# Kernel optimization log

Hardware: AMD Instinct MI355X
Metric: run time of the kernel (lower is better)

## Reference

```python
import jax, jax.numpy as jnp
import numpy as np

D_IN, D, TOPK = 64, 4, 12
SCALE = 1.0 / np.sqrt(np.float32(D_IN))


def setup_inputs() -> dict:
    key = jax.random.key(0)
    kx, kw = jax.random.split(key)
    x = jax.random.normal(kx, (8, 16, 512, D_IN), dtype=jnp.float32)
    flat = jax.random.normal(kw, (2 * D_IN * D,), dtype=jnp.float32)
    return {"x": x, "flat": flat}


def reference(x, flat):
    # x: (N, T, n, d_in); flat holds wk then wq, each (d_in, d)
    wk = flat[: D_IN * D].reshape(D_IN, D)
    wq = flat[D_IN * D :].reshape(D_IN, D)
    N, T, n, _ = x.shape
    k = jnp.einsum("btnc,cd->btnd", x, wk)  # (N,T,n,d)
    q = jnp.einsum("btnc,cd->btnd", x, wq)  # (N,T,n,d)
    # h = (X Wk)(X Wq)^T : h[i,j] = k_i . q_j -> (N,T,n,n)
    h = jnp.einsum("btnd,btmd->btnm", k, q)
    A = jax.nn.softmax(SCALE * h, axis=-1).sum(axis=-2)  # (N,T,n) column score sums
    # argsort descending + slice topk == top_k indices (values sorted descending)
    _, idxs = jax.lax.top_k(A, TOPK)  # (N,T,topk)
    return idxs.reshape(N, T, TOPK, 1)
```

## Files before the change

### kernel.cpp

```cpp
#include <hip/hip_runtime.h>
#include <math.h>

constexpr int kDIn  = 64;
constexpr int kN    = 512;
constexpr int kTopK = 12;
constexpr int kNBt  = 128;
constexpr int kS    = 4;
constexpr int kRows = kN / kS;
#define CEXP 0.18033688f
#define EXP2(v) __builtin_amdgcn_exp2f(v)
#define LOG2F(v) __builtin_amdgcn_logf(v)

#define DOT4(k, q)        fmaf((k).x,(q).x, fmaf((k).y,(q).y, fmaf((k).z,(q).z, (k).w*(q).w)))
#define DOT4A(k, q, add)  fmaf((k).x,(q).x, fmaf((k).y,(q).y, fmaf((k).z,(q).z, fmaf((k).w,(q).w,(add)))))

constexpr size_t kWsFloats = (size_t)kNBt * 16 * kN;

__global__ __launch_bounds__(512, 4) void fused_attn_kernel(
    const float* __restrict__ x, const float* __restrict__ flat,
    float* __restrict__ apart)
{
  __shared__ float4 Qs[kN];
  __shared__ float4 Ks[kRows];
  __shared__ float2 Pp[16 * kRows];
  __shared__ __align__(16) float Cs[kRows];

  const int tid  = threadIdx.x;
  const int p    = blockIdx.x;
  const int xcd  = p & 7;
  const int s    = (p >> 3) & 3;
  const int tile = ((p >> 5) << 3) | xcd;

  {
    const float4* fw  = reinterpret_cast<const float4*>(flat);
    const float4* xr4 = reinterpret_cast<const float4*>(x + ((size_t)tile * kN + tid) * kDIn);
    float4 xv[16];
#pragma unroll
    for (int i = 0; i < 16; ++i) xv[i] = xr4[i];

    float q0=0.f,q1=0.f,q2=0.f,q3=0.f;
    if ((tid >> 7) == s) {
      float k0=0.f,k1=0.f,k2=0.f,k3=0.f;
#pragma unroll
      for (int cc = 0; cc < 16; ++cc) {
#pragma unroll
        for (int u = 0; u < 4; ++u) {
          float v = (u==0)?xv[cc].x:(u==1)?xv[cc].y:(u==2)?xv[cc].z:xv[cc].w;
          float4 a = fw[cc*4+u];
          float4 b = fw[64 + cc*4+u];
          k0 = fmaf(v, a.x, k0); k1 = fmaf(v, a.y, k1);
          k2 = fmaf(v, a.z, k2); k3 = fmaf(v, a.w, k3);
          q0 = fmaf(v, b.x, q0); q1 = fmaf(v, b.y, q1);
          q2 = fmaf(v, b.z, q2); q3 = fmaf(v, b.w, q3);
        }
      }
      Ks[tid & 127] = make_float4(CEXP*k0, CEXP*k1, CEXP*k2, CEXP*k3);
    } else {
#pragma unroll
      for (int cc = 0; cc < 16; ++cc) {
#pragma unroll
        for (int u = 0; u < 4; ++u) {
          float v = (u==0)?xv[cc].x:(u==1)?xv[cc].y:(u==2)?xv[cc].z:xv[cc].w;
          float4 b = fw[64 + cc*4+u];
          q0 = fmaf(v, b.x, q0); q1 = fmaf(v, b.y, q1);
          q2 = fmaf(v, b.z, q2); q3 = fmaf(v, b.w, q3);
        }
      }
    }
    Qs[tid] = make_float4(q0, q1, q2, q3);
  }
  __syncthreads();

  {
    const int quad  = tid & 31;
    const int slice = tid >> 5;
    const float4 k0 = Ks[quad*4+0], k1 = Ks[quad*4+1];
    const float4 k2 = Ks[quad*4+2], k3 = Ks[quad*4+3];
    const float4* qb = &Qs[slice << 5];

    float m0=-INFINITY, m1=-INFINITY, m2=-INFINITY, m3=-INFINITY;
    float l0=0.f, l1=0.f, l2=0.f, l3=0.f;
#pragma unroll
    for (int c = 0; c < 32; c += 8) {
      float4 qv0 = qb[c+0], qv1 = qb[c+1], qv2 = qb[c+2], qv3 = qb[c+3];
      float4 qv4 = qb[c+4], qv5 = qb[c+5], qv6 = qb[c+6], qv7 = qb[c+7];
#define ROW_ONLINE(KR, MR, LR)                                                 \
      {                                                                        \
        float d0 = DOT4(KR, qv0), d1 = DOT4(KR, qv1);                          \
        float d2 = DOT4(KR, qv2), d3 = DOT4(KR, qv3);                          \
        float d4 = DOT4(KR, qv4), d5 = DOT4(KR, qv5);                          \
        float d6 = DOT4(KR, qv6), d7 = DOT4(KR, qv7);                          \
        float cm = fmaxf(fmaxf(fmaxf(d0,d1), fmaxf(d2,d3)),                    \
                         fmaxf(fmaxf(d4,d5), fmaxf(d6,d7)));                   \
        if (cm > MR) { LR *= EXP2(MR - cm); MR = cm; }                         \
        LR += ((EXP2(d0-MR) + EXP2(d1-MR)) + (EXP2(d2-MR) + EXP2(d3-MR)))      \
            + ((EXP2(d4-MR) + EXP2(d5-MR)) + (EXP2(d6-MR) + EXP2(d7-MR)));     \
      }
      ROW_ONLINE(k0, m0, l0)
      ROW_ONLINE(k1, m1, l1)
      ROW_ONLINE(k2, m2, l2)
      ROW_ONLINE(k3, m3, l3)
#undef ROW_ONLINE
    }
    float4* pp4 = reinterpret_cast<float4*>(&Pp[slice * kRows + quad*4]);
    pp4[0] = make_float4(m0, l0, m1, l1);
    pp4[1] = make_float4(m2, l2, m3, l3);
  }
  __syncthreads();

  if (tid < kRows) {
    float m = -INFINITY;
    float2 pr[16];
#pragma unroll
    for (int sl = 0; sl < 16; ++sl) {
      pr[sl] = Pp[sl * kRows + tid];
      m = fmaxf(m, pr[sl].x);
    }
    float l = 0.f;
#pragma unroll
    for (int sl = 0; sl < 16; ++sl) l += pr[sl].y * EXP2(pr[sl].x - m);
    Cs[tid] = m + LOG2F(l);
  }
  __syncthreads();

  {
    const int cq = tid & 127;
    const int rs = tid >> 7;
    const float4 q0 = Qs[cq*4+0], q1 = Qs[cq*4+1];
    const float4 q2 = Qs[cq*4+2], q3 = Qs[cq*4+3];
    const float4* kb = &Ks[rs << 5];
    const float4* cb = reinterpret_cast<const float4*>(&Cs[rs << 5]);

    float a0=0.f, a1=0.f, a2=0.f, a3=0.f;
#pragma unroll 2
    for (int ii = 0; ii < 8; ++ii) {
      float4 cc = cb[ii];
      float4 ka = kb[ii*4+0], kb_ = kb[ii*4+1], kc = kb[ii*4+2], kd = kb[ii*4+3];
      a0 += EXP2(DOT4A(q0, ka, -cc.x));  a1 += EXP2(DOT4A(q1, ka, -cc.x));
      a2 += EXP2(DOT4A(q2, ka, -cc.x));  a3 += EXP2(DOT4A(q3, ka, -cc.x));
      a0 += EXP2(DOT4A(q0, kb_, -cc.y)); a1 += EXP2(DOT4A(q1, kb_, -cc.y));
      a2 += EXP2(DOT4A(q2, kb_, -cc.y)); a3 += EXP2(DOT4A(q3, kb_, -cc.y));
      a0 += EXP2(DOT4A(q0, kc, -cc.z));  a1 += EXP2(DOT4A(q1, kc, -cc.z));
      a2 += EXP2(DOT4A(q2, kc, -cc.z));  a3 += EXP2(DOT4A(q3, kc, -cc.z));
      a0 += EXP2(DOT4A(q0, kd, -cc.w));  a1 += EXP2(DOT4A(q1, kd, -cc.w));
      a2 += EXP2(DOT4A(q2, kd, -cc.w));  a3 += EXP2(DOT4A(q3, kd, -cc.w));
    }
    reinterpret_cast<float4*>(apart + ((size_t)(tile*4 + s) * 4 + rs) * kN)[cq] =
        make_float4(a0, a1, a2, a3);
  }
}

__global__ __launch_bounds__(64) void topk_kernel(
    const float* __restrict__ apart, int* __restrict__ out)
{
  const int lane = threadIdx.x;
  const int bt   = blockIdx.x;
  const float* P = apart + (size_t)bt * 16 * kN;

  float v[8];
  {
    float4 acc0 = make_float4(0.f,0.f,0.f,0.f);
    float4 acc1 = make_float4(0.f,0.f,0.f,0.f);
#pragma unroll
    for (int sl = 0; sl < 16; ++sl) {
      const float4* Ps = reinterpret_cast<const float4*>(P + sl * kN);
      float4 u0 = Ps[lane*2], u1 = Ps[lane*2+1];
      acc0.x += u0.x; acc0.y += u0.y; acc0.z += u0.z; acc0.w += u0.w;
      acc1.x += u1.x; acc1.y += u1.y; acc1.z += u1.z; acc1.w += u1.w;
    }
    v[0]=acc0.x; v[1]=acc0.y; v[2]=acc0.z; v[3]=acc0.w;
    v[4]=acc1.x; v[5]=acc1.y; v[6]=acc1.z; v[7]=acc1.w;
  }

  for (int rnd = 0; rnd < kTopK; ++rnd) {
    float bv = v[0];
    int   bi = lane * 8;
#pragma unroll
    for (int r = 1; r < 8; ++r) {
      if (v[r] > bv) { bv = v[r]; bi = lane * 8 + r; }
    }
#pragma unroll
    for (int off = 32; off >= 1; off >>= 1) {
      float ov = __shfl_xor(bv, off);
      int   oi = __shfl_xor(bi, off);
      if (ov > bv || (ov == bv && oi < bi)) { bv = ov; bi = oi; }
    }
    if (lane == 0) out[bt * kTopK + rnd] = bi;
#pragma unroll
    for (int r = 0; r < 8; ++r) {
      if (lane * 8 + r == bi) v[r] = -INFINITY;
    }
  }
}

__global__ __launch_bounds__(512, 1) void sparse_attn_topk_fallback(
    const float* __restrict__ x, const float* __restrict__ flat, int* __restrict__ out)
{
  __shared__ float4 wk4[kDIn];
  __shared__ float4 wq4[kDIn];
  __shared__ float4 Ks[kN];
  __shared__ float4 Qs[kN];
  __shared__ float  Ms[kN];
  __shared__ float  Rl[kN];
  __shared__ float  As[kN];

  const int tid = threadIdx.x;
  const int bt  = blockIdx.x;

  if (tid < 64)       wk4[tid]      = reinterpret_cast<const float4*>(flat)[tid];
  else if (tid < 128) wq4[tid - 64] = reinterpret_cast<const float4*>(flat)[tid];
  __syncthreads();

  const float* xr = x + ((size_t)bt * kN + tid) * kDIn;
  float k0=0.f,k1=0.f,k2=0.f,k3=0.f, q0=0.f,q1=0.f,q2=0.f,q3=0.f;
#pragma unroll
  for (int c = 0; c < kDIn; ++c) {
    float xv = xr[c];
    float4 a = wk4[c];
    float4 b = wq4[c];
    k0 = fmaf(xv, a.x, k0); k1 = fmaf(xv, a.y, k1);
    k2 = fmaf(xv, a.z, k2); k3 = fmaf(xv, a.w, k3);
    q0 = fmaf(xv, b.x, q0); q1 = fmaf(xv, b.y, q1);
    q2 = fmaf(xv, b.z, q2); q3 = fmaf(xv, b.w, q3);
  }
  Ks[tid] = make_float4(k0, k1, k2, k3);
  Qs[tid] = make_float4(q0, q1, q2, q3);
  __syncthreads();

  float m = -INFINITY;
#pragma unroll 8
  for (int j = 0; j < kN; ++j) {
    float4 qj = Qs[j];
    float h = fmaf(k0, qj.x, fmaf(k1, qj.y, fmaf(k2, qj.z, k3 * qj.w)));
    m = fmaxf(m, h);
  }
  float l = 0.f;
#pragma unroll 8
  for (int j = 0; j < kN; ++j) {
    float4 qj = Qs[j];
    float h = fmaf(k0, qj.x, fmaf(k1, qj.y, fmaf(k2, qj.z, k3 * qj.w)));
    l += exp2f(CEXP * (h - m));
  }
  Ms[tid] = m;
  Rl[tid] = 1.0f / l;
  __syncthreads();

  float acc = 0.f;
#pragma unroll 8
  for (int i = 0; i < kN; ++i) {
    float4 ki = Ks[i];
    float h = fmaf(q0, ki.x, fmaf(q1, ki.y, fmaf(q2, ki.z, q3 * ki.w)));
    acc += exp2f(CEXP * (h - Ms[i])) * Rl[i];
  }
  As[tid] = acc;
  __syncthreads();

  if (tid < 64) {
    float v[8];
#pragma unroll
    for (int r = 0; r < 8; ++r) v[r] = As[tid * 8 + r];
    for (int rnd = 0; rnd < kTopK; ++rnd) {
      float bv = v[0];
      int   bi = tid * 8;
#pragma unroll
      for (int r = 1; r < 8; ++r)
        if (v[r] > bv) { bv = v[r]; bi = tid * 8 + r; }
#pragma unroll
      for (int off = 32; off >= 1; off >>= 1) {
        float ov = __shfl_xor(bv, off);
        int   oi = __shfl_xor(bi, off);
        if (ov > bv || (ov == bv && oi < bi)) { bv = ov; bi = oi; }
      }
      if (tid == 0) out[bt * kTopK + rnd] = bi;
#pragma unroll
      for (int r = 0; r < 8; ++r)
        if (tid * 8 + r == bi) v[r] = -INFINITY;
    }
  }
}

extern "C" void kernel_launch(void* const* d_in, const int* in_sizes, int n_in,
                              void* d_out, int out_size, void* d_ws, size_t ws_size,
                              hipStream_t stream) {
  const float* x    = (const float*)d_in[0];
  const float* flat = (const float*)d_in[1];
  int* out = (int*)d_out;
  const int n_bt = in_sizes[0] / (kN * kDIn);

  if (n_bt != kNBt || ws_size < kWsFloats * sizeof(float)) {
    sparse_attn_topk_fallback<<<n_bt, kN, 0, stream>>>(x, flat, out);
    return;
  }
  float* apart = (float*)d_ws;
  fused_attn_kernel<<<kNBt * kS, 512, 0, stream>>>(x, flat, apart);
  topk_kernel      <<<kNBt,       64, 0, stream>>>(apart, out);
}
```

Before: 36.65 us.

## Fuse top-k into attention kernel via last-arriving-block atomic counter

Removes the separate topk_kernel launch. Each attention block increments a per-tile atomic counter after a threadfence, and the last of the four split blocks for a tile reduces the partial column sums and selects the top-k indices. This saves a kernel launch and the gap between kernels. In exchange it adds a hipMemsetAsync to reset the counters, plus fences and atomics in every block.

New measurement: 113.0 us. 3.08x slower.

```diff
diff --git a/kernel.cpp b/kernel.cpp
--- a/kernel.cpp
+++ b/kernel.cpp
@@ -14,16 +14,19 @@
 #define DOT4(k, q)        fmaf((k).x,(q).x, fmaf((k).y,(q).y, fmaf((k).z,(q).z, (k).w*(q).w)))
 #define DOT4A(k, q, add)  fmaf((k).x,(q).x, fmaf((k).y,(q).y, fmaf((k).z,(q).z, fmaf((k).w,(q).w,(add)))))
 
-constexpr size_t kWsFloats = (size_t)kNBt * 16 * kN;
+constexpr size_t kApFloats = (size_t)kNBt * 16 * kN;
+constexpr size_t kWsBytes  = kApFloats * 4 + kNBt * 4;
 
 __global__ __launch_bounds__(512, 4) void fused_attn_kernel(
     const float* __restrict__ x, const float* __restrict__ flat,
-    float* __restrict__ apart)
+    float* __restrict__ apart, int* __restrict__ counters,
+    int* __restrict__ out)
 {
   __shared__ float4 Qs[kN];
   __shared__ float4 Ks[kRows];
   __shared__ float2 Pp[16 * kRows];
   __shared__ __align__(16) float Cs[kRows];
+  __shared__ int lastArr;
 
   const int tid  = threadIdx.x;
   const int p    = blockIdx.x;
@@ -148,47 +151,52 @@
     reinterpret_cast<float4*>(apart + ((size_t)(tile*4 + s) * 4 + rs) * kN)[cq] =
         make_float4(a0, a1, a2, a3);
   }
-}
-
-__global__ __launch_bounds__(64) void topk_kernel(
-    const float* __restrict__ apart, int* __restrict__ out)
-{
-  const int lane = threadIdx.x;
-  const int bt   = blockIdx.x;
-  const float* P = apart + (size_t)bt * 16 * kN;
-
-  float v[8];
-  {
-    float4 acc0 = make_float4(0.f,0.f,0.f,0.f);
-    float4 acc1 = make_float4(0.f,0.f,0.f,0.f);
-#pragma unroll
-    for (int sl = 0; sl < 16; ++sl) {
-      const float4* Ps = reinterpret_cast<const float4*>(P + sl * kN);
-      float4 u0 = Ps[lane*2], u1 = Ps[lane*2+1];
-      acc0.x += u0.x; acc0.y += u0.y; acc0.z += u0.z; acc0.w += u0.w;
-      acc1.x += u1.x; acc1.y += u1.y; acc1.z += u1.z; acc1.w += u1.w;
-    }
-    v[0]=acc0.x; v[1]=acc0.y; v[2]=acc0.z; v[3]=acc0.w;
-    v[4]=acc1.x; v[5]=acc1.y; v[6]=acc1.z; v[7]=acc1.w;
-  }
-
-  for (int rnd = 0; rnd < kTopK; ++rnd) {
-    float bv = v[0];
-    int   bi = lane * 8;
-#pragma unroll
-    for (int r = 1; r < 8; ++r) {
-      if (v[r] > bv) { bv = v[r]; bi = lane * 8 + r; }
-    }
-#pragma unroll
-    for (int off = 32; off >= 1; off >>= 1) {
-      float ov = __shfl_xor(bv, off);
-      int   oi = __shfl_xor(bi, off);
-      if (ov > bv || (ov == bv && oi < bi)) { bv = ov; bi = oi; }
-    }
-    if (lane == 0) out[bt * kTopK + rnd] = bi;
-#pragma unroll
-    for (int r = 0; r < 8; ++r) {
-      if (lane * 8 + r == bi) v[r] = -INFINITY;
+
+  __threadfence();
+  if (tid == 0) {
+    int old = atomicAdd(&counters[tile], 1);
+    lastArr = (old == 3);
+  }
+  __syncthreads();
+
+  if (lastArr && tid < 64) {
+    __threadfence();
+    const int lane = tid;
+    const float* P = apart + (size_t)tile * 16 * kN;
+
+    float v[8];
+    {
+      float4 acc0 = make_float4(0.f,0.f,0.f,0.f);
+      float4 acc1 = make_float4(0.f,0.f,0.f,0.f);
+#pragma unroll
+      for (int sl = 0; sl < 16; ++sl) {
+        const float4* Ps = reinterpret_cast<const float4*>(P + sl * kN);
+        float4 u0 = Ps[lane*2], u1 = Ps[lane*2+1];
+        acc0.x += u0.x; acc0.y += u0.y; acc0.z += u0.z; acc0.w += u0.w;
+        acc1.x += u1.x; acc1.y += u1.y; acc1.z += u1.z; acc1.w += u1.w;
+      }
+      v[0]=acc0.x; v[1]=acc0.y; v[2]=acc0.z; v[3]=acc0.w;
+      v[4]=acc1.x; v[5]=acc1.y; v[6]=acc1.z; v[7]=acc1.w;
+    }
+
+    for (int rnd = 0; rnd < kTopK; ++rnd) {
+      float bv = v[0];
+      int   bi = lane * 8;
+#pragma unroll
+      for (int r = 1; r < 8; ++r) {
+        if (v[r] > bv) { bv = v[r]; bi = lane * 8 + r; }
+      }
+#pragma unroll
+      for (int off = 32; off >= 1; off >>= 1) {
+        float ov = __shfl_xor(bv, off);
+        int   oi = __shfl_xor(bi, off);
+        if (ov > bv || (ov == bv && oi < bi)) { bv = ov; bi = oi; }
+      }
+      if (lane == 0) out[tile * kTopK + rnd] = bi;
+#pragma unroll
+      for (int r = 0; r < 8; ++r) {
+        if (lane * 8 + r == bi) v[r] = -INFINITY;
+      }
     }
   }
 }
@@ -287,11 +295,13 @@
   int* out = (int*)d_out;
   const int n_bt = in_sizes[0] / (kN * kDIn);
 
-  if (n_bt != kNBt || ws_size < kWsFloats * sizeof(float)) {
+  if (n_bt != kNBt || ws_size < kWsBytes) {
     sparse_attn_topk_fallback<<<n_bt, kN, 0, stream>>>(x, flat, out);
     return;
   }
-  float* apart = (float*)d_ws;
-  fused_attn_kernel<<<kNBt * kS, 512, 0, stream>>>(x, flat, apart);
-  topk_kernel      <<<kNBt,       64, 0, stream>>>(apart, out);
+  float* apart   = (float*)d_ws;
+  int*   counters = (int*)((char*)d_ws + kApFloats * 4);
+
+  hipMemsetAsync(counters, 0, kNBt * sizeof(int), stream);
+  fused_attn_kernel<<<kNBt * kS, 512, 0, stream>>>(x, flat, apart, counters, out);
 }
```

## Merge softmax row statistics with wavefront shuffles instead of shared-memory pass

Applied to the files above, without the earlier changes.

Reassigns threads so the 16 column slices of each row group sit in adjacent lanes, then merges the online max/sum partials with xor shuffles. This removes the Pp shared buffer, one __syncthreads, and the serial 128-thread merge phase. Q in shared memory gets padding (one float4 every 32 entries) so the new slice-strided access pattern avoids bank conflicts. Launch bounds now target 6 blocks per CU, which can raise occupancy but caps registers per thread more tightly and risks spills.

Measured after the change: 37.34 us. About the same (+1.9%).

```diff
diff --git a/kernel.cpp b/kernel.cpp
--- a/kernel.cpp
+++ b/kernel.cpp
@@ -14,15 +14,16 @@
 #define DOT4(k, q)        fmaf((k).x,(q).x, fmaf((k).y,(q).y, fmaf((k).z,(q).z, (k).w*(q).w)))
 #define DOT4A(k, q, add)  fmaf((k).x,(q).x, fmaf((k).y,(q).y, fmaf((k).z,(q).z, fmaf((k).w,(q).w,(add)))))
 
+#define QIDX(j) ((j) + ((j) >> 5))
+
 constexpr size_t kWsFloats = (size_t)kNBt * 16 * kN;
 
-__global__ __launch_bounds__(512, 4) void fused_attn_kernel(
+__global__ __launch_bounds__(512, 6) void fused_attn_kernel(
     const float* __restrict__ x, const float* __restrict__ flat,
     float* __restrict__ apart)
 {
-  __shared__ float4 Qs[kN];
+  __shared__ float4 Qs[kN + 16];
   __shared__ float4 Ks[kRows];
-  __shared__ float2 Pp[16 * kRows];
   __shared__ __align__(16) float Cs[kRows];
 
   const int tid  = threadIdx.x;
@@ -67,16 +68,16 @@
         }
       }
     }
-    Qs[tid] = make_float4(q0, q1, q2, q3);
+    Qs[QIDX(tid)] = make_float4(q0, q1, q2, q3);
   }
   __syncthreads();
 
   {
-    const int quad  = tid & 31;
-    const int slice = tid >> 5;
+    const int quad  = tid >> 4;
+    const int slice = tid & 15;
     const float4 k0 = Ks[quad*4+0], k1 = Ks[quad*4+1];
     const float4 k2 = Ks[quad*4+2], k3 = Ks[quad*4+3];
-    const float4* qb = &Qs[slice << 5];
+    const float4* qb = &Qs[slice * 33];
 
     float m0=-INFINITY, m1=-INFINITY, m2=-INFINITY, m3=-INFINITY;
     float l0=0.f, l1=0.f, l2=0.f, l3=0.f;
@@ -102,32 +103,34 @@
       ROW_ONLINE(k3, m3, l3)
 #undef ROW_ONLINE
     }
-    float4* pp4 = reinterpret_cast<float4*>(&Pp[slice * kRows + quad*4]);
-    pp4[0] = make_float4(m0, l0, m1, l1);
-    pp4[1] = make_float4(m2, l2, m3, l3);
-  }
-  __syncthreads();
-
-  if (tid < kRows) {
-    float m = -INFINITY;
-    float2 pr[16];
-#pragma unroll
-    for (int sl = 0; sl < 16; ++sl) {
-      pr[sl] = Pp[sl * kRows + tid];
-      m = fmaxf(m, pr[sl].x);
-    }
-    float l = 0.f;
-#pragma unroll
-    for (int sl = 0; sl < 16; ++sl) l += pr[sl].y * EXP2(pr[sl].x - m);
-    Cs[tid] = m + LOG2F(l);
+#pragma unroll
+    for (int off = 1; off <= 8; off <<= 1) {
+#define MERGE(MR, LR)                                                          \
+      {                                                                        \
+        float om = __shfl_xor(MR, off);                                        \
+        float ol = __shfl_xor(LR, off);                                        \
+        float nm = fmaxf(MR, om);                                              \
+        LR = fmaf(LR, EXP2(MR - nm), ol * EXP2(om - nm));                      \
+        MR = nm;                                                               \
+      }
+      MERGE(m0, l0)
+      MERGE(m1, l1)
+      MERGE(m2, l2)
+      MERGE(m3, l3)
+#undef MERGE
+    }
+    if (slice == 0) {
+      *reinterpret_cast<float4*>(&Cs[quad*4]) = make_float4(
+          m0 + LOG2F(l0), m1 + LOG2F(l1), m2 + LOG2F(l2), m3 + LOG2F(l3));
+    }
   }
   __syncthreads();
 
   {
     const int cq = tid & 127;
     const int rs = tid >> 7;
-    const float4 q0 = Qs[cq*4+0], q1 = Qs[cq*4+1];
-    const float4 q2 = Qs[cq*4+2], q3 = Qs[cq*4+3];
+    const float4 q0 = Qs[QIDX(cq*4+0)], q1 = Qs[QIDX(cq*4+1)];
+    const float4 q2 = Qs[QIDX(cq*4+2)], q3 = Qs[QIDX(cq*4+3)];
     const float4* kb = &Ks[rs << 5];
     const float4* cb = reinterpret_cast<const float4*>(&Cs[rs << 5]);
 
```
